# Performance work log

Hardware: AMD Instinct MI355X
Metric: run time of the kernel (lower is better)

## Reference

```python
import jax, jax.numpy as jnp
import numpy as np

SHAPES = ((64, 64), (32, 32), (16, 16), (8, 8))
LEVEL_STARTS = np.concatenate([[0], np.cumsum([h * w for h, w in SHAPES])]).tolist()
N_LEVELS = 4; N_HEADS = 8; N_POINTS = 4; D_MODEL = 256; HEAD_DIM = 32; D_FFN = 1024; NUM_LAYERS = 2
LEN_IN = sum(h * w for h, w in SHAPES)
BATCH = 2


def setup_inputs():
    key = jax.random.key(0)
    ks = iter(jax.random.split(key, 40))
    r = lambda shape, s=1.0: jax.random.normal(next(ks), shape, dtype=jnp.float32) * s
    L = NUM_LAYERS
    return {
        "src": r((BATCH, LEN_IN, D_MODEL)),
        "pos": r((BATCH, LEN_IN, D_MODEL), 0.5),
        "valid_ratios": jnp.ones((BATCH, N_LEVELS, 2), jnp.float32),
        "Wv": r((L, D_MODEL, D_MODEL), 0.05), "bv": jnp.zeros((L, D_MODEL), jnp.float32),
        "Woff": r((L, D_MODEL, N_HEADS * N_LEVELS * N_POINTS * 2), 0.002),
        "boff": r((L, N_HEADS * N_LEVELS * N_POINTS * 2), 0.5),
        "Wa": r((L, D_MODEL, N_HEADS * N_LEVELS * N_POINTS), 0.05),
        "ba": jnp.zeros((L, N_HEADS * N_LEVELS * N_POINTS), jnp.float32),
        "Wo": r((L, D_MODEL, D_MODEL), 0.05), "bo": jnp.zeros((L, D_MODEL), jnp.float32),
        "g1": jnp.ones((L, D_MODEL), jnp.float32), "be1": jnp.zeros((L, D_MODEL), jnp.float32),
        "Wl1": r((L, D_MODEL, D_FFN), 0.05), "bl1": jnp.zeros((L, D_FFN), jnp.float32),
        "Wl2": r((L, D_FFN, D_MODEL), 0.05), "bl2": jnp.zeros((L, D_MODEL), jnp.float32),
        "g2": jnp.ones((L, D_MODEL), jnp.float32), "be2": jnp.zeros((L, D_MODEL), jnp.float32),
    }


def layer_norm(x, g, b, eps=1e-5):
    m = jnp.mean(x, -1, keepdims=True)
    v = jnp.mean(jnp.square(x - m), -1, keepdims=True)
    return (x - m) * jax.lax.rsqrt(v + eps) * g + b


def make_reference_points(valid_ratios):
    # DeformableTransformerEncoder.get_reference_points, vectorized per level
    refs = []
    for lvl, (H, W) in enumerate(SHAPES):
        gy, gx = jnp.meshgrid(jnp.arange(H, dtype=jnp.float32) + 0.5,
                              jnp.arange(W, dtype=jnp.float32) + 0.5, indexing="ij")
        ry = gy.reshape(-1)[None] / (valid_ratios[:, lvl, 1][:, None] * H)
        rx = gx.reshape(-1)[None] / (valid_ratios[:, lvl, 0][:, None] * W)
        refs.append(jnp.stack([rx, ry], -1))  # [N, H*W, 2]
    ref = jnp.concatenate(refs, 1)  # [N, Len, 2]
    return ref[:, :, None, :] * valid_ratios[:, None]  # [N, Len, n_levels, 2]


def ms_deform_attn(query, input_flatten, reference_points, Wv, bv, Woff, boff, Wa, ba, Wo, bo):
    N, Lq, _ = query.shape
    value = (input_flatten @ Wv + bv).reshape(N, -1, N_HEADS, HEAD_DIM)
    off = (query @ Woff + boff).reshape(N, Lq, N_HEADS, N_LEVELS, N_POINTS, 2)
    aw = (query @ Wa + ba).reshape(N, Lq, N_HEADS, N_LEVELS * N_POINTS)
    aw = jax.nn.softmax(aw, -1).reshape(N, Lq, N_HEADS, N_LEVELS, N_POINTS)
    # normalizer is (W, H) per level, as in MSDeformAttn
    normalizer = jnp.array([[w, h] for h, w in SHAPES], jnp.float32)
    loc = reference_points[:, :, None, :, None, :] + off / normalizer[None, None, None, :, None, :]
    acc = jnp.zeros((N, N_HEADS, Lq, HEAD_DIM), query.dtype)
    for lvl, (H, W) in enumerate(SHAPES):
        s = LEVEL_STARTS[lvl]
        val = value[:, s:s + H * W].transpose(0, 2, 1, 3)  # [N, heads, H*W, hd]
        # grid_sample bilinear, align_corners=False, zero padding
        x = loc[:, :, :, lvl, :, 0] * W - 0.5  # [N, Lq, heads, P]
        y = loc[:, :, :, lvl, :, 1] * H - 0.5
        x0 = jnp.floor(x); y0 = jnp.floor(y)
        wx1 = x - x0; wy1 = y - y0
        ix0 = x0.astype(jnp.int32); iy0 = y0.astype(jnp.int32)

        def corner(ix, iy, w):
            valid = (ix >= 0) & (ix < W) & (iy >= 0) & (iy < H)
            idx = jnp.clip(iy, 0, H - 1) * W + jnp.clip(ix, 0, W - 1)
            idx = idx.transpose(0, 2, 1, 3).reshape(N, N_HEADS, Lq * N_POINTS)
            g = jnp.take_along_axis(val, idx[..., None], axis=2).reshape(N, N_HEADS, Lq, N_POINTS, HEAD_DIM)
            w = jnp.where(valid, w, 0.0).transpose(0, 2, 1, 3)  # [N, heads, Lq, P]
            return g * w[..., None]

        sampled = (corner(ix0, iy0, (1 - wx1) * (1 - wy1))
                   + corner(ix0 + 1, iy0, wx1 * (1 - wy1))
                   + corner(ix0, iy0 + 1, (1 - wx1) * wy1)
                   + corner(ix0 + 1, iy0 + 1, wx1 * wy1))
        acc = acc + (sampled * aw[:, :, :, lvl].transpose(0, 2, 1, 3)[..., None]).sum(3)
    out = acc.transpose(0, 2, 1, 3).reshape(N, Lq, D_MODEL)
    return out @ Wo + bo


def reference(src, pos, valid_ratios, Wv, bv, Woff, boff, Wa, ba, Wo, bo,
              g1, be1, Wl1, bl1, Wl2, bl2, g2, be2):
    ref_pts = make_reference_points(valid_ratios)
    out = src
    for l in range(NUM_LAYERS):
        q = out + pos  # with_pos_embed
        attn = ms_deform_attn(q, out, ref_pts, Wv[l], bv[l], Woff[l], boff[l],
                              Wa[l], ba[l], Wo[l], bo[l])
        out = layer_norm(out + attn, g1[l], be1[l])
        ffn = jax.nn.relu(out @ Wl1[l] + bl1[l]) @ Wl2[l] + bl2[l]
        out = layer_norm(out + ffn, g2[l], be2[l])
    return out
```

## Files before the change

kernel.cpp:

```cpp
#include <hip/hip_runtime.h>
#include <math.h>

#define LEN   5440
#define NB    2
#define MROWS (NB * LEN)
#define DM    256
#define NH    8
#define HD    32
#define NLV   4
#define NPT   4
#define DFFN  1024

typedef __attribute__((ext_vector_type(8))) short bf16x8;
typedef __attribute__((ext_vector_type(4))) short bf16x4;
typedef __attribute__((ext_vector_type(4))) float f32x4;

#define MFMA16 __builtin_amdgcn_mfma_f32_16x16x32_bf16

__device__ __forceinline__ short f2bf(float f) {
    union { float f; unsigned u; } cv; cv.f = f;
    unsigned r = cv.u + 0x7fffu + ((cv.u >> 16) & 1u);
    return (short)(r >> 16);
}
__device__ __forceinline__ float bf2f(short s) {
    union { unsigned u; float f; } cv;
    cv.u = ((unsigned)(unsigned short)s) << 16;
    return cv.f;
}

__device__ __forceinline__ void gload16(const short* g, short* l) {
    __builtin_amdgcn_global_load_lds(
        (__attribute__((address_space(1))) void*)g,
        (__attribute__((address_space(3))) void*)l, 16, 0, 0);
}

template <int N> __device__ __forceinline__ void vmwait();
template <> __device__ __forceinline__ void vmwait<0>() { asm volatile("s_waitcnt vmcnt(0)" ::: "memory"); }
template <> __device__ __forceinline__ void vmwait<4>() { asm volatile("s_waitcnt vmcnt(4)" ::: "memory"); }
template <> __device__ __forceinline__ void vmwait<5>() { asm volatile("s_waitcnt vmcnt(5)" ::: "memory"); }

__device__ __forceinline__ int swz(int row) { return (row >> 1) & 3; }

__global__ __launch_bounds__(256) void transpose_convert_all(
    const float* __restrict__ Wv,  const float* __restrict__ Woff,
    const float* __restrict__ Wa,  const float* __restrict__ Wo,
    const float* __restrict__ Wl1, const float* __restrict__ Wl2,
    short* __restrict__ out)
{
    int bx = blockIdx.x;
    int l  = bx / 736;
    int t  = bx % 736;
    const float* src; int K, N; long doff;
    if      (t < 64)  { src = Wv;   K = 256;  N = 256;  doff = 0;      }
    else if (t < 128) { src = Woff; K = 256;  N = 256;  doff = 65536;  t -= 64;  }
    else if (t < 160) { src = Wa;   K = 256;  N = 128;  doff = 131072; t -= 128; }
    else if (t < 224) { src = Wo;   K = 256;  N = 256;  doff = 163840; t -= 160; }
    else if (t < 480) { src = Wl1;  K = 256;  N = 1024; doff = 229376; t -= 224; }
    else              { src = Wl2;  K = 1024; N = 256;  doff = 491520; t -= 480; }
    src += (long)l * K * N;
    short* dst = out + (long)l * 753664 + doff;

    const int ntx = N / 32;
    const int n0 = (t % ntx) * 32, k0 = (t / ntx) * 32;

    __shared__ short T[32][33];
    const int tid = threadIdx.x;
    {
        const int n = tid & 31, kq = tid >> 5;
        #pragma unroll
        for (int i = 0; i < 4; ++i) {
            int k = kq * 4 + i;
            T[n][k] = f2bf(src[(long)(k0 + k) * N + n0 + n]);
        }
    }
    __syncthreads();
    {
        const int k = tid & 31, nq = tid >> 5;
        #pragma unroll
        for (int i = 0; i < 4; ++i) {
            int n = nq * 4 + i;
            dst[(long)(n0 + n) * K + k0 + k] = T[n][k];
        }
    }
}

__global__ __launch_bounds__(256) void convert_src(
    const float4* __restrict__ s4, const float4* __restrict__ p4,
    bf16x4* __restrict__ curb, bf16x4* __restrict__ qb)
{
    const int i = blockIdx.x * 256 + threadIdx.x;
    float4 s = s4[i], p = p4[i];
    bf16x4 c, q;
    c[0] = f2bf(s.x); c[1] = f2bf(s.y); c[2] = f2bf(s.z); c[3] = f2bf(s.w);
    q[0] = f2bf(s.x + p.x); q[1] = f2bf(s.y + p.y);
    q[2] = f2bf(s.z + p.z); q[3] = f2bf(s.w + p.w);
    curb[i] = c; qb[i] = q;
}

template <int RELU, int OMODE, int K>
__device__ __forceinline__ void gemm_core128_v2(
    short* As, short* Bs,
    const short* __restrict__ A, const short* __restrict__ Wt,
    const float* __restrict__ bias, float* __restrict__ Cf,
    short* __restrict__ Cb, int ldc, int m0, int wrow0, int ccol0)
{
    constexpr int NT = K / 32;
    static_assert(NT >= 4 && (NT & 1) == 0, "NT even >= 4");
    const int t    = threadIdx.x;
    const int wave = t >> 6, lane = t & 63;
    const int wm   = (wave & 1) * 64;
    const int wn   = (wave >> 1) * 64;
    const int lm   = lane & 15;
    const int chkg = lane >> 4;

    const short* aS[2]; const short* bS[2];
    short *aD[2], *bD[2];
    #pragma unroll
    for (int i = 0; i < 2; ++i) {
        const int c   = wave * 2 + i;
        const int row = c * 16 + (lane >> 2);
        const int xc  = (lane & 3) ^ swz(row);
        aS[i] = A  + (long)(m0 + row) * K + xc * 8;
        bS[i] = Wt + (long)(wrow0 + row) * K + xc * 8;
        aD[i] = As + c * 512;
        bD[i] = Bs + c * 512;
    }

    int offA[4], offB[4];
    #pragma unroll
    for (int s = 0; s < 4; ++s) {
        const int r = wm + s * 16 + lm;
        offA[s] = r * 32 + (chkg ^ swz(r)) * 8;
    }
    #pragma unroll
    for (int u = 0; u < 4; ++u) {
        const int r = wn + u * 16 + lm;
        offB[u] = r * 32 + (chkg ^ swz(r)) * 8;
    }

    f32x4 acc[4][4] = {};

#define STG128(BUF, KT) do {                                          \
        const int _ko = (KT) * 32;                                    \
        gload16(aS[0] + _ko, aD[0] + (BUF) * 4096);                   \
        gload16(bS[0] + _ko, bD[0] + (BUF) * 4096);                   \
        gload16(aS[1] + _ko, aD[1] + (BUF) * 4096);                   \
        gload16(bS[1] + _ko, bD[1] + (BUF) * 4096);                   \
    } while (0)

#define GB128(T, BUF, WN, DOSTAGE) do {                               \
        vmwait<WN>();                     \
        __builtin_amdgcn_s_barrier();     \
        bf16x8 af[4], bv[4];                                          \
        _Pragma("unroll")                                             \
        for (int s = 0; s < 4; ++s)                                   \
            af[s] = *(const bf16x8*)(As + (BUF) * 4096 + offA[s]);    \
        _Pragma("unroll")                                             \
        for (int u = 0; u < 4; ++u)                                   \
            bv[u] = *(const bf16x8*)(Bs + (BUF) * 4096 + offB[u]);    \
        asm volatile("s_waitcnt lgkmcnt(0)" ::: "memory");            \
        __builtin_amdgcn_s_barrier();     \
        __builtin_amdgcn_sched_barrier(0);                            \
        if (DOSTAGE) STG128(BUF, (T) + 2);                            \
        _Pragma("unroll")                                             \
        for (int s = 0; s < 4; ++s)                                   \
            _Pragma("unroll")                                         \
            for (int u = 0; u < 4; ++u)                               \
                acc[s][u] = MFMA16(af[s], bv[u], acc[s][u], 0, 0, 0); \
    } while (0)

    STG128(0, 0);
    STG128(1, 1);
    for (int tt = 0; tt < NT - 2; tt += 2) {
        GB128(tt,     0, 4, true);
        GB128(tt + 1, 1, 4, true);
    }
    GB128(NT - 2, 0, 4, false);
    GB128(NT - 1, 1, 0, false);
#undef GB128
#undef STG128

    const int col = lane & 15;
    const int rq  = (lane >> 4) * 4;
    #pragma unroll
    for (int s = 0; s < 4; ++s) {
        #pragma unroll
        for (int u = 0; u < 4; ++u) {
            const int gn = ccol0 + wn + u * 16 + col;
            const float bb = bias[gn];
            #pragma unroll
            for (int r = 0; r < 4; ++r) {
                const int gm = m0 + wm + s * 16 + rq + r;
                float v = acc[s][u][r] + bb;
                if (RELU) v = fmaxf(v, 0.f);
                if (OMODE == 0) {
                    Cf[(long)gm * ldc + gn] = v;
                } else if (OMODE == 1) {
                    Cb[(long)gm * ldc + gn] = f2bf(v);
                } else {
                    const int n   = gm / LEN;
                    const int pix = gm - n * LEN;
                    const int h   = gn >> 5, d = gn & 31;
                    Cb[((long)(n * NH + h) * LEN + pix) * 32 + d] = f2bf(v);
                }
            }
        }
    }
}

template <int RELU, int OMODE, int K>
__global__ __launch_bounds__(256) void gemm128v2(
    const short* __restrict__ A, const short* __restrict__ Wt,
    const float* __restrict__ bias, float* Cf, short* Cb, int ldc)
{
    __shared__ __align__(16) short As[2 * 128 * 32];
    __shared__ __align__(16) short Bs[2 * 128 * 32];
    gemm_core128_v2<RELU, OMODE, K>(As, Bs, A, Wt, bias, Cf, Cb, ldc,
                                    blockIdx.y * 128, blockIdx.x * 128,
                                    blockIdx.x * 128);
}

__global__ __launch_bounds__(256) void gemm_qkv128(
    const short* __restrict__ curb, const short* __restrict__ qb,
    const short* __restrict__ Wt, const float* __restrict__ bv,
    const float* __restrict__ boff, const float* __restrict__ ba,
    short* __restrict__ Vb, float* __restrict__ OFF, float* __restrict__ AW)
{
    __shared__ __align__(16) short As[2 * 128 * 32];
    __shared__ __align__(16) short Bs[2 * 128 * 32];
    const int n0 = blockIdx.x * 128;
    if (n0 < 256) {
        gemm_core128_v2<0, 2, 256>(As, Bs, curb, Wt, bv, (float*)nullptr, Vb,
                                   256, blockIdx.y * 128, n0, n0);
    } else if (n0 < 512) {
        gemm_core128_v2<0, 0, 256>(As, Bs, qb, Wt, boff, OFF, (short*)nullptr,
                                   256, blockIdx.y * 128, n0, n0 - 256);
    } else {
        gemm_core128_v2<0, 0, 256>(As, Bs, qb, Wt, ba, AW, (short*)nullptr,
                                   128, blockIdx.y * 128, n0, n0 - 512);
    }
}

template <int K>
__global__ __launch_bounds__(256) void gemm_ln(
    const short* __restrict__ A, const short* __restrict__ Wt,
    const float* __restrict__ bias, const short* __restrict__ residb,
    const float* __restrict__ g, const float* __restrict__ be,
    short* __restrict__ outb, short* __restrict__ outq,
    float* __restrict__ outf, const float* __restrict__ pos)
{
    constexpr int NT = K / 32;
    __shared__ __align__(16) short As[2 * 32 * 32];
    __shared__ __align__(16) short Bs[2 * 256 * 32];
    __shared__ float red[2][32][2];

    const int t    = threadIdx.x;
    const int wave = t >> 6, lane = t & 63;
    const int wm   = (wave & 1) * 16;
    const int wn   = (wave >> 1) * 128;
    const int lm   = lane & 15;
    const int chkg = lane >> 4;
    const int rq   = chkg * 4;
    const int m0   = blockIdx.x * 32;
    const bool hasA = (wave & 1) == 0;

    short rr[8][4];
    #pragma unroll
    for (int u = 0; u < 8; ++u)
        #pragma unroll
        for (int r = 0; r < 4; ++r)
            rr[u][r] = residb[(long)(m0 + wm + rq + r) * DM + wn + u * 16 + lm];
    asm volatile("" ::: "memory");

    const short* bSp[4]; short* bDp[4];
    #pragma unroll
    for (int i = 0; i < 4; ++i) {
        const int c   = wave * 4 + i;
        const int row = c * 16 + (lane >> 2);
        const int xc  = (lane & 3) ^ swz(row);
        bSp[i] = Wt + (long)row * K + xc * 8;
        bDp[i] = Bs + c * 512;
    }
    const short* aSp = nullptr; short* aDp = nullptr;
    if (hasA) {
        const int c   = wave >> 1;
        const int row = c * 16 + (lane >> 2);
        const int xc  = (lane & 3) ^ swz(row);
        aSp = A + (long)(m0 + row) * K + xc * 8;
        aDp = As + c * 512;
    }

    const int offA = (wm + lm) * 32 + (chkg ^ swz(wm + lm)) * 8;
    int offB[8];
    #pragma unroll
    for (int u = 0; u < 8; ++u) {
        const int r = wn + u * 16 + lm;
        offB[u] = r * 32 + (chkg ^ swz(r)) * 8;
    }

    f32x4 acc[8] = {};

#define STGLN(BUF, KT) do {                                           \
        const int _ko = (KT) * 32;                                    \
        if (hasA) gload16(aSp + _ko, aDp + (BUF) * 1024);             \
        gload16(bSp[0] + _ko, bDp[0] + (BUF) * 8192);                 \
        gload16(bSp[1] + _ko, bDp[1] + (BUF) * 8192);                 \
        gload16(bSp[2] + _ko, bDp[2] + (BUF) * 8192);                 \
        gload16(bSp[3] + _ko, bDp[3] + (BUF) * 8192);                 \
    } while (0)

#define GBLN(T, BUF, WA, WB, DOSTAGE) do {                            \
        if (hasA) vmwait<WA>(); else vmwait<WB>();                    \
        __builtin_amdgcn_s_barrier();                                 \
        bf16x8 af = *(const bf16x8*)(As + (BUF) * 1024 + offA);       \
        bf16x8 bv[8];                                                 \
        _Pragma("unroll")                                             \
        for (int u = 0; u < 8; ++u)                                   \
            bv[u] = *(const bf16x8*)(Bs + (BUF) * 8192 + offB[u]);    \
        asm volatile("s_waitcnt lgkmcnt(0)" ::: "memory");            \
        __builtin_amdgcn_s_barrier();                                 \
        __builtin_amdgcn_sched_barrier(0);                            \
        if (DOSTAGE) STGLN(BUF, (T) + 2);                             \
        _Pragma("unroll")                                             \
        for (int u = 0; u < 8; ++u)                                   \
            acc[u] = MFMA16(af, bv[u], acc[u], 0, 0, 0);              \
    } while (0)

    STGLN(0, 0);
    STGLN(1, 1);
    for (int tt = 0; tt < NT - 2; tt += 2) {
        GBLN(tt,     0, 5, 4, true);
        GBLN(tt + 1, 1, 5, 4, true);
    }
    GBLN(NT - 2, 0, 5, 4, false);
    GBLN(NT - 1, 1, 0, 0, false);
#undef GBLN
#undef STGLN

    #pragma unroll
    for (int u = 0; u < 8; ++u) {
        const int gn = wn + u * 16 + lm;
        const float bb = bias[gn];
        #pragma unroll
        for (int r = 0; r < 4; ++r)
            acc[u][r] += bb + bf2f(rr[u][r]);
    }

    float rs[4], r2[4];
    #pragma unroll
    for (int r = 0; r < 4; ++r) {
        float s = 0.f, s2 = 0.f;
        #pragma unroll
        for (int u = 0; u < 8; ++u) { const float v = acc[u][r]; s += v; s2 += v * v; }
        rs[r] = s; r2[r] = s2;
    }
    #pragma unroll
    for (int o = 1; o < 16; o <<= 1)
        #pragma unroll
        for (int r = 0; r < 4; ++r) {
            rs[r] += __shfl_xor(rs[r], o, 64);
            r2[r] += __shfl_xor(r2[r], o, 64);
        }
    if (lm == 0) {
        #pragma unroll
        for (int r = 0; r < 4; ++r) {
            red[wave >> 1][wm + rq + r][0] = rs[r];
            red[wave >> 1][wm + rq + r][1] = r2[r];
        }
    }
    __syncthreads();
    #pragma unroll
    for (int r = 0; r < 4; ++r) {
        const int row = wm + rq + r;
        const float ts = red[0][row][0] + red[1][row][0];
        const float t2 = red[0][row][1] + red[1][row][1];
        const float mean = ts * (1.f / DM);
        const float var  = t2 * (1.f / DM) - mean * mean;
        rs[r] = mean;
        r2[r] = rsqrtf(var + 1e-5f);
    }
    #pragma unroll
    for (int u = 0; u < 8; ++u) {
        const int gn = wn + u * 16 + lm;
        const float gg = g[gn], bbe = be[gn];
        #pragma unroll
        for (int r = 0; r < 4; ++r) {
            const long gm = m0 + wm + rq + r;
            const float o = (acc[u][r] - rs[r]) * r2[r] * gg + bbe;
            if (outb) outb[gm * DM + gn] = f2bf(o);
            if (outq) outq[gm * DM + gn] = f2bf(o + pos[gm * DM + gn]);
            if (outf) outf[gm * DM + gn] = o;
        }
    }
}

__global__ __launch_bounds__(256) void deform_attn_v3(
    const short* __restrict__ Vb,
    const float* __restrict__ OFF,
    const float* __restrict__ AW,
    const float* __restrict__ vr,
    bf16x4* __restrict__ ATTb)
{
    const int starts[5] = {0, 4096, 5120, 5376, 5440};
    const int dims[4]   = {64, 32, 16, 8};

    const int wave = threadIdx.x >> 6;
    const int lane = threadIdx.x & 63;
    const int h    = lane >> 3;
    const int d4   = lane & 7;

    const int gq = blockIdx.x * 4 + wave;
    const int n  = gq / LEN;
    const int q  = gq % LEN;

    int lq = 3;
    if (q < 4096) lq = 0; else if (q < 5120) lq = 1; else if (q < 5376) lq = 2;
    const int r  = q - starts[lq];
    const int Wq = dims[lq];
    const int gy = r / Wq, gx = r % Wq;
    const float vrxq = vr[(n * NLV + lq) * 2 + 0];
    const float vryq = vr[(n * NLV + lq) * 2 + 1];
    const float rx = (gx + 0.5f) / (vrxq * Wq);
    const float ry = (gy + 0.5f) / (vryq * Wq);

    const long row = (long)n * LEN + q;

    const float* awp = AW + row * 128 + h * 16;
    float a[16];
    float mx = -1e30f;
    #pragma unroll
    for (int i = 0; i < 16; ++i) { a[i] = awp[i]; mx = fmaxf(mx, a[i]); }
    float s = 0.f;
    #pragma unroll
    for (int i = 0; i < 16; ++i) { a[i] = __expf(a[i] - mx); s += a[i]; }
    const float inv = 1.f / s;

    const float* offp = OFF + row * 256 + h * 32;

    float4 acc = {0.f, 0.f, 0.f, 0.f};
    #pragma unroll
    for (int lvl = 0; lvl < NLV; ++lvl) {
        const int Hl = dims[lvl];
        const int Wl = Hl;
        const float fW = (float)Wl;
        const int sb = starts[lvl];
        const float lx = rx * vr[(n * NLV + lvl) * 2 + 0];
        const float ly = ry * vr[(n * NLV + lvl) * 2 + 1];
        const short* vb = Vb + ((long)(n * NH + h) * LEN + sb) * 32 + d4 * 4;
        #pragma unroll
        for (int p = 0; p < NPT; ++p) {
            const float ox = offp[lvl * 8 + p * 2 + 0];
            const float oy = offp[lvl * 8 + p * 2 + 1];
            const float x = fmaf(lx, fW, ox) - 0.5f;
            const float y = fmaf(ly, fW, oy) - 0.5f;
            const float x0f = floorf(x), y0f = floorf(y);
            const int ix0 = (int)x0f, iy0 = (int)y0f;
            const float wx1 = x - x0f, wy1 = y - y0f;
            const float wx0 = 1.f - wx1, wy0 = 1.f - wy1;

            const bool vx0 = (ix0 >= 0)     && (ix0 < Wl);
            const bool vx1 = (ix0 + 1 >= 0) && (ix0 + 1 < Wl);
            const bool vy0 = (iy0 >= 0)     && (iy0 < Hl);
            const bool vy1 = (iy0 + 1 >= 0) && (iy0 + 1 < Hl);
            const int cx0 = min(max(ix0, 0), Wl - 1);
            const int cx1 = min(max(ix0 + 1, 0), Wl - 1);
            const int cy0 = min(max(iy0, 0), Hl - 1);
            const int cy1 = min(max(iy0 + 1, 0), Hl - 1);

            const float w00 = (vx0 && vy0) ? wx0 * wy0 : 0.f;
            const float w10 = (vx1 && vy0) ? wx1 * wy0 : 0.f;
            const float w01 = (vx0 && vy1) ? wx0 * wy1 : 0.f;
            const float w11 = (vx1 && vy1) ? wx1 * wy1 : 0.f;

            const bf16x4 g00 = *(const bf16x4*)(vb + (long)(cy0 * Wl + cx0) * 32);
            const bf16x4 g10 = *(const bf16x4*)(vb + (long)(cy0 * Wl + cx1) * 32);
            const bf16x4 g01 = *(const bf16x4*)(vb + (long)(cy1 * Wl + cx0) * 32);
            const bf16x4 g11 = *(const bf16x4*)(vb + (long)(cy1 * Wl + cx1) * 32);

            const float awv = a[lvl * 4 + p] * inv;
            #pragma unroll
            for (int e = 0; e < 4; ++e) {
                float sv = w00 * bf2f(g00[e]) + w10 * bf2f(g10[e])
                         + w01 * bf2f(g01[e]) + w11 * bf2f(g11[e]);
                (&acc.x)[e] += awv * sv;
            }
        }
    }
    bf16x4 ob;
    ob[0] = f2bf(acc.x); ob[1] = f2bf(acc.y);
    ob[2] = f2bf(acc.z); ob[3] = f2bf(acc.w);
    ATTb[row * 64 + h * 8 + d4] = ob;
}

extern "C" void kernel_launch(void* const* d_in, const int* in_sizes, int n_in,
                              void* d_out, int out_size, void* d_ws, size_t ws_size,
                              hipStream_t stream)
{
    const float* src = (const float*)d_in[0];
    const float* pos = (const float*)d_in[1];
    const float* vr  = (const float*)d_in[2];
    const float* Wv_   = (const float*)d_in[3];
    const float* bv_   = (const float*)d_in[4];
    const float* Woff_ = (const float*)d_in[5];
    const float* boff_ = (const float*)d_in[6];
    const float* Wa_   = (const float*)d_in[7];
    const float* ba_   = (const float*)d_in[8];
    const float* Wo_   = (const float*)d_in[9];
    const float* bo_   = (const float*)d_in[10];
    const float* g1_   = (const float*)d_in[11];
    const float* be1_  = (const float*)d_in[12];
    const float* Wl1_  = (const float*)d_in[13];
    const float* bl1_  = (const float*)d_in[14];
    const float* Wl2_  = (const float*)d_in[15];
    const float* bl2_  = (const float*)d_in[16];
    const float* g2_   = (const float*)d_in[17];
    const float* be2_  = (const float*)d_in[18];

    const long SZ = (long)MROWS * DM;
    float* ws = (float*)d_ws;
    float* OFF  = ws;
    float* AW   = OFF + SZ;
    short* Vb   = (short*)(AW + (long)MROWS * 128);
    short* curb = Vb   + SZ;
    short* qb   = curb + SZ;
    short* ATTb = qb   + SZ;
    short* XAb  = ATTb + SZ;
    short* FFNb = XAb  + SZ;
    short* Wt   = FFNb + (long)MROWS * DFFN;

    const dim3 blk(256);
    const int GYM = MROWS / 128;
    const int GLN = MROWS / 32;

    hipLaunchKernelGGL(transpose_convert_all, dim3(1472), blk, 0, stream,
                       Wv_, Woff_, Wa_, Wo_, Wl1_, Wl2_, Wt);
    hipLaunchKernelGGL(convert_src, dim3(SZ / 4 / 256), blk, 0, stream,
                       (const float4*)src, (const float4*)pos,
                       (bf16x4*)curb, (bf16x4*)qb);

    for (int l = 0; l < 2; ++l) {
        const short* Wbase = Wt + (long)l * 753664;
        const float* bv   = bv_   + (long)l * DM;
        const float* boff = boff_ + (long)l * 256;
        const float* ba   = ba_   + (long)l * 128;
        const float* bo   = bo_   + (long)l * DM;
        const float* g1   = g1_   + (long)l * DM;
        const float* be1  = be1_  + (long)l * DM;
        const float* bl1  = bl1_  + (long)l * DFFN;
        const float* bl2  = bl2_  + (long)l * DM;
        const float* g2   = g2_   + (long)l * DM;
        const float* be2  = be2_  + (long)l * DM;

        hipLaunchKernelGGL(gemm_qkv128, dim3(5, GYM), blk, 0, stream,
                           curb, qb, Wbase, bv, boff, ba, Vb, OFF, AW);
        hipLaunchKernelGGL(deform_attn_v3, dim3(MROWS / 4), blk, 0, stream,
                           Vb, OFF, AW, vr, (bf16x4*)ATTb);
        hipLaunchKernelGGL((gemm_ln<256>), dim3(GLN), blk, 0, stream,
                           ATTb, Wbase + 163840, bo, curb, g1, be1,
                           XAb, (short*)nullptr, (float*)nullptr,
                           (const float*)nullptr);
        hipLaunchKernelGGL((gemm128v2<1, 1, 256>), dim3(8, GYM), blk, 0, stream,
                           XAb, Wbase + 229376, bl1, (float*)nullptr, FFNb, 1024);
        if (l == 0) {
            hipLaunchKernelGGL((gemm_ln<1024>), dim3(GLN), blk, 0, stream,
                               FFNb, Wbase + 491520, bl2, XAb, g2, be2,
                               curb, qb, (float*)nullptr, pos);
        } else {
            hipLaunchKernelGGL((gemm_ln<1024>), dim3(GLN), blk, 0, stream,
                               FFNb, Wbase + 491520, bl2, XAb, g2, be2,
                               (short*)nullptr, (short*)nullptr,
                               (float*)d_out, (const float*)nullptr);
        }
    }
}
```

Before: 291.9 us.

## Use 4-slot LDS ring with register double-buffering in GEMM main loops; merge prep kernels

```diff
diff --git a/kernel.cpp b/kernel.cpp
--- a/kernel.cpp
+++ b/kernel.cpp
@@ -39,14 +39,32 @@
 template <> __device__ __forceinline__ void vmwait<4>() { asm volatile("s_waitcnt vmcnt(4)" ::: "memory"); }
 template <> __device__ __forceinline__ void vmwait<5>() { asm volatile("s_waitcnt vmcnt(5)" ::: "memory"); }
 
+template <int N> __device__ __forceinline__ void lgkwait();
+template <> __device__ __forceinline__ void lgkwait<0>() { asm volatile("s_waitcnt lgkmcnt(0)" ::: "memory"); }
+template <> __device__ __forceinline__ void lgkwait<8>() { asm volatile("s_waitcnt lgkmcnt(8)" ::: "memory"); }
+template <> __device__ __forceinline__ void lgkwait<9>() { asm volatile("s_waitcnt lgkmcnt(9)" ::: "memory"); }
+
 __device__ __forceinline__ int swz(int row) { return (row >> 1) & 3; }
 
-__global__ __launch_bounds__(256) void transpose_convert_all(
+__global__ __launch_bounds__(256) void prep_all(
     const float* __restrict__ Wv,  const float* __restrict__ Woff,
     const float* __restrict__ Wa,  const float* __restrict__ Wo,
     const float* __restrict__ Wl1, const float* __restrict__ Wl2,
-    short* __restrict__ out)
+    short* __restrict__ out,
+    const float4* __restrict__ s4, const float4* __restrict__ p4,
+    bf16x4* __restrict__ curb, bf16x4* __restrict__ qb)
 {
+    __shared__ short T[32][33];
+    if (blockIdx.x >= 1472) {
+        const int i = (blockIdx.x - 1472) * 256 + threadIdx.x;
+        float4 s = s4[i], p = p4[i];
+        bf16x4 c, q;
+        c[0] = f2bf(s.x); c[1] = f2bf(s.y); c[2] = f2bf(s.z); c[3] = f2bf(s.w);
+        q[0] = f2bf(s.x + p.x); q[1] = f2bf(s.y + p.y);
+        q[2] = f2bf(s.z + p.z); q[3] = f2bf(s.w + p.w);
+        curb[i] = c; qb[i] = q;
+        return;
+    }
     int bx = blockIdx.x;
     int l  = bx / 736;
     int t  = bx % 736;
@@ -63,7 +81,6 @@
     const int ntx = N / 32;
     const int n0 = (t % ntx) * 32, k0 = (t / ntx) * 32;
 
-    __shared__ short T[32][33];
     const int tid = threadIdx.x;
     {
         const int n = tid & 31, kq = tid >> 5;
@@ -84,28 +101,15 @@
     }
 }
 
-__global__ __launch_bounds__(256) void convert_src(
-    const float4* __restrict__ s4, const float4* __restrict__ p4,
-    bf16x4* __restrict__ curb, bf16x4* __restrict__ qb)
-{
-    const int i = blockIdx.x * 256 + threadIdx.x;
-    float4 s = s4[i], p = p4[i];
-    bf16x4 c, q;
-    c[0] = f2bf(s.x); c[1] = f2bf(s.y); c[2] = f2bf(s.z); c[3] = f2bf(s.w);
-    q[0] = f2bf(s.x + p.x); q[1] = f2bf(s.y + p.y);
-    q[2] = f2bf(s.z + p.z); q[3] = f2bf(s.w + p.w);
-    curb[i] = c; qb[i] = q;
-}
-
 template <int RELU, int OMODE, int K>
-__device__ __forceinline__ void gemm_core128_v2(
+__device__ __forceinline__ void gemm_core128_v3(
     short* As, short* Bs,
     const short* __restrict__ A, const short* __restrict__ Wt,
     const float* __restrict__ bias, float* __restrict__ Cf,
     short* __restrict__ Cb, int ldc, int m0, int wrow0, int ccol0)
 {
     constexpr int NT = K / 32;
-    static_assert(NT >= 4 && (NT & 1) == 0, "NT even >= 4");
+    static_assert(NT >= 4, "NT >= 4");
     const int t    = threadIdx.x;
     const int wave = t >> 6, lane = t & 63;
     const int wm   = (wave & 1) * 64;
@@ -139,46 +143,56 @@
     }
 
     f32x4 acc[4][4] = {};
-
-#define STG128(BUF, KT) do {                                          \
+    bf16x8 afr[2][4], bfr[2][4];
+
+#define STG3(KT) do {                                                 \
+        const int _b  = ((KT) & 3) * 4096;                            \
         const int _ko = (KT) * 32;                                    \
-        gload16(aS[0] + _ko, aD[0] + (BUF) * 4096);                   \
-        gload16(bS[0] + _ko, bD[0] + (BUF) * 4096);                   \
-        gload16(aS[1] + _ko, aD[1] + (BUF) * 4096);                   \
-        gload16(bS[1] + _ko, bD[1] + (BUF) * 4096);                   \
+        gload16(aS[0] + _ko, aD[0] + _b);                             \
+        gload16(bS[0] + _ko, bD[0] + _b);                             \
+        gload16(aS[1] + _ko, aD[1] + _b);                             \
+        gload16(bS[1] + _ko, bD[1] + _b);                             \
     } while (0)
 
-#define GB128(T, BUF, WN, DOSTAGE) do {                               \
-        vmwait<WN>();                     \
-        __builtin_amdgcn_s_barrier();     \
-        bf16x8 af[4], bv[4];                                          \
+#define RD3(SET, KT) do {                                             \
+        const int _b = ((KT) & 3) * 4096;                             \
         _Pragma("unroll")                                             \
         for (int s = 0; s < 4; ++s)                                   \
-            af[s] = *(const bf16x8*)(As + (BUF) * 4096 + offA[s]);    \
+            afr[SET][s] = *(const bf16x8*)(As + _b + offA[s]);        \
         _Pragma("unroll")                                             \
         for (int u = 0; u < 4; ++u)                                   \
-            bv[u] = *(const bf16x8*)(Bs + (BUF) * 4096 + offB[u]);    \
-        asm volatile("s_waitcnt lgkmcnt(0)" ::: "memory");            \
-        __builtin_amdgcn_s_barrier();     \
-        __builtin_amdgcn_sched_barrier(0);                            \
-        if (DOSTAGE) STG128(BUF, (T) + 2);                            \
-        _Pragma("unroll")                                             \
-        for (int s = 0; s < 4; ++s)                                   \
-            _Pragma("unroll")                                         \
-            for (int u = 0; u < 4; ++u)                               \
-                acc[s][u] = MFMA16(af[s], bv[u], acc[s][u], 0, 0, 0); \
+            bfr[SET][u] = *(const bf16x8*)(Bs + _b + offB[u]);        \
     } while (0)
 
-    STG128(0, 0);
-    STG128(1, 1);
-    for (int tt = 0; tt < NT - 2; tt += 2) {
-        GB128(tt,     0, 4, true);
-        GB128(tt + 1, 1, 4, true);
-    }
-    GB128(NT - 2, 0, 4, false);
-    GB128(NT - 1, 1, 0, false);
-#undef GB128
-#undef STG128
+    STG3(0);
+    STG3(1);
+    vmwait<4>();
+    __builtin_amdgcn_s_barrier();
+    RD3(0, 0);
+
+    #pragma unroll
+    for (int kt = 0; kt < NT; ++kt) {
+        if (kt + 2 < NT) STG3(kt + 2);
+        if (kt + 1 < NT) {
+            if (kt + 2 < NT) vmwait<4>(); else vmwait<0>();
+            __builtin_amdgcn_s_barrier();
+            RD3((kt + 1) & 1, kt + 1);
+            lgkwait<8>();
+        } else {
+            lgkwait<0>();
+        }
+        __builtin_amdgcn_sched_barrier(0);
+        __builtin_amdgcn_s_setprio(1);
+        const int cs = kt & 1;
+        #pragma unroll
+        for (int s = 0; s < 4; ++s)
+            #pragma unroll
+            for (int u = 0; u < 4; ++u)
+                acc[s][u] = MFMA16(afr[cs][s], bfr[cs][u], acc[s][u], 0, 0, 0);
+        __builtin_amdgcn_s_setprio(0);
+    }
+#undef RD3
+#undef STG3
 
     const int col = lane & 15;
     const int rq  = (lane >> 4) * 4;
@@ -209,13 +223,13 @@
 }
 
 template <int RELU, int OMODE, int K>
-__global__ __launch_bounds__(256) void gemm128v2(
+__global__ __launch_bounds__(256) void gemm128v3(
     const short* __restrict__ A, const short* __restrict__ Wt,
     const float* __restrict__ bias, float* Cf, short* Cb, int ldc)
 {
-    __shared__ __align__(16) short As[2 * 128 * 32];
-    __shared__ __align__(16) short Bs[2 * 128 * 32];
-    gemm_core128_v2<RELU, OMODE, K>(As, Bs, A, Wt, bias, Cf, Cb, ldc,
+    __shared__ __align__(16) short As[4 * 128 * 32];
+    __shared__ __align__(16) short Bs[4 * 128 * 32];
+    gemm_core128_v3<RELU, OMODE, K>(As, Bs, A, Wt, bias, Cf, Cb, ldc,
                                     blockIdx.y * 128, blockIdx.x * 128,
                                     blockIdx.x * 128);
 }
@@ -226,17 +240,17 @@
     const float* __restrict__ boff, const float* __restrict__ ba,
     short* __restrict__ Vb, float* __restrict__ OFF, float* __restrict__ AW)
 {
-    __shared__ __align__(16) short As[2 * 128 * 32];
-    __shared__ __align__(16) short Bs[2 * 128 * 32];
+    __shared__ __align__(16) short As[4 * 128 * 32];
+    __shared__ __align__(16) short Bs[4 * 128 * 32];
     const int n0 = blockIdx.x * 128;
     if (n0 < 256) {
-        gemm_core128_v2<0, 2, 256>(As, Bs, curb, Wt, bv, (float*)nullptr, Vb,
+        gemm_core128_v3<0, 2, 256>(As, Bs, curb, Wt, bv, (float*)nullptr, Vb,
                                    256, blockIdx.y * 128, n0, n0);
     } else if (n0 < 512) {
-        gemm_core128_v2<0, 0, 256>(As, Bs, qb, Wt, boff, OFF, (short*)nullptr,
+        gemm_core128_v3<0, 0, 256>(As, Bs, qb, Wt, boff, OFF, (short*)nullptr,
                                    256, blockIdx.y * 128, n0, n0 - 256);
     } else {
-        gemm_core128_v2<0, 0, 256>(As, Bs, qb, Wt, ba, AW, (short*)nullptr,
+        gemm_core128_v3<0, 0, 256>(As, Bs, qb, Wt, ba, AW, (short*)nullptr,
                                    128, blockIdx.y * 128, n0, n0 - 512);
     }
 }
@@ -250,8 +264,8 @@
     float* __restrict__ outf, const float* __restrict__ pos)
 {
     constexpr int NT = K / 32;
-    __shared__ __align__(16) short As[2 * 32 * 32];
-    __shared__ __align__(16) short Bs[2 * 256 * 32];
+    __shared__ __align__(16) short As[4 * 32 * 32];
+    __shared__ __align__(16) short Bs[4 * 256 * 32];
     __shared__ float red[2][32][2];
 
     const int t    = threadIdx.x;
@@ -299,43 +313,56 @@
     }
 
     f32x4 acc[8] = {};
-
-#define STGLN(BUF, KT) do {                                           \
+    bf16x8 afr[2], bfr[2][8];
+
+#define STGL(KT) do {                                                 \
+        const int _ba = ((KT) & 3) * 1024;                            \
+        const int _bb = ((KT) & 3) * 8192;                            \
         const int _ko = (KT) * 32;                                    \
-        if (hasA) gload16(aSp + _ko, aDp + (BUF) * 1024);             \
-        gload16(bSp[0] + _ko, bDp[0] + (BUF) * 8192);                 \
-        gload16(bSp[1] + _ko, bDp[1] + (BUF) * 8192);                 \
-        gload16(bSp[2] + _ko, bDp[2] + (BUF) * 8192);                 \
-        gload16(bSp[3] + _ko, bDp[3] + (BUF) * 8192);                 \
+        if (hasA) gload16(aSp + _ko, aDp + _ba);                      \
+        gload16(bSp[0] + _ko, bDp[0] + _bb);                          \
+        gload16(bSp[1] + _ko, bDp[1] + _bb);                          \
+        gload16(bSp[2] + _ko, bDp[2] + _bb);                          \
+        gload16(bSp[3] + _ko, bDp[3] + _bb);                          \
     } while (0)
 
-#define GBLN(T, BUF, WA, WB, DOSTAGE) do {                            \
-        if (hasA) vmwait<WA>(); else vmwait<WB>();                    \
-        __builtin_amdgcn_s_barrier();                                 \
-        bf16x8 af = *(const bf16x8*)(As + (BUF) * 1024 + offA);       \
-        bf16x8 bv[8];                                                 \
+#define RDL(SET, KT) do {                                             \
+        const int _ba = ((KT) & 3) * 1024;                            \
+        const int _bb = ((KT) & 3) * 8192;                            \
+        afr[SET] = *(const bf16x8*)(As + _ba + offA);                 \
         _Pragma("unroll")                                             \
         for (int u = 0; u < 8; ++u)                                   \
-            bv[u] = *(const bf16x8*)(Bs + (BUF) * 8192 + offB[u]);    \
-        asm volatile("s_waitcnt lgkmcnt(0)" ::: "memory");            \
-        __builtin_amdgcn_s_barrier();                                 \
-        __builtin_amdgcn_sched_barrier(0);                            \
-        if (DOSTAGE) STGLN(BUF, (T) + 2);                             \
-        _Pragma("unroll")                                             \
-        for (int u = 0; u < 8; ++u)                                   \
-            acc[u] = MFMA16(af, bv[u], acc[u], 0, 0, 0);              \
+            bfr[SET][u] = *(const bf16x8*)(Bs + _bb + offB[u]);       \
     } while (0)
 
-    STGLN(0, 0);
-    STGLN(1, 1);
-    for (int tt = 0; tt < NT - 2; tt += 2) {
-        GBLN(tt,     0, 5, 4, true);
-        GBLN(tt + 1, 1, 5, 4, true);
-    }
-    GBLN(NT - 2, 0, 5, 4, false);
-    GBLN(NT - 1, 1, 0, 0, false);
-#undef GBLN
-#undef STGLN
+    STGL(0);
+    STGL(1);
+    if (hasA) vmwait<5>(); else vmwait<4>();
+    __builtin_amdgcn_s_barrier();
+    RDL(0, 0);
+
+    #pragma unroll
+    for (int kt = 0; kt < NT; ++kt) {
+        if (kt + 2 < NT) STGL(kt + 2);
+        if (kt + 1 < NT) {
+            if (kt + 2 < NT) { if (hasA) vmwait<5>(); else vmwait<4>(); }
+            else             vmwait<0>();
+            __builtin_amdgcn_s_barrier();
+            RDL((kt + 1) & 1, kt + 1);
+            lgkwait<9>();
+        } else {
+            lgkwait<0>();
+        }
+        __builtin_amdgcn_sched_barrier(0);
+        __builtin_amdgcn_s_setprio(1);
+        const int cs = kt & 1;
+        #pragma unroll
+        for (int u = 0; u < 8; ++u)
+            acc[u] = MFMA16(afr[cs], bfr[cs][u], acc[u], 0, 0, 0);
+        __builtin_amdgcn_s_setprio(0);
+    }
+#undef RDL
+#undef STGL
 
     #pragma unroll
     for (int u = 0; u < 8; ++u) {
@@ -532,9 +559,8 @@
     const int GYM = MROWS / 128;
     const int GLN = MROWS / 32;
 
-    hipLaunchKernelGGL(transpose_convert_all, dim3(1472), blk, 0, stream,
-                       Wv_, Woff_, Wa_, Wo_, Wl1_, Wl2_, Wt);
-    hipLaunchKernelGGL(convert_src, dim3(SZ / 4 / 256), blk, 0, stream,
+    hipLaunchKernelGGL(prep_all, dim3(1472 + SZ / 4 / 256), blk, 0, stream,
+                       Wv_, Woff_, Wa_, Wo_, Wl1_, Wl2_, Wt,
                        (const float4*)src, (const float4*)pos,
                        (bf16x4*)curb, (bf16x4*)qb);
 
@@ -559,7 +585,7 @@
                            ATTb, Wbase + 163840, bo, curb, g1, be1,
                            XAb, (short*)nullptr, (float*)nullptr,
                            (const float*)nullptr);
-        hipLaunchKernelGGL((gemm128v2<1, 1, 256>), dim3(8, GYM), blk, 0, stream,
+        hipLaunchKernelGGL((gemm128v3<1, 1, 256>), dim3(8, GYM), blk, 0, stream,
                            XAb, Wbase + 229376, bl1, (float*)nullptr, FFNb, 1024);
         if (l == 0) {
             hipLaunchKernelGGL((gemm_ln<1024>), dim3(GLN), blk, 0, stream,
```

Measured after the change: 297.4 us. Within noise of the previous version (+1.9%).

## Split-K the FFN second GEMM with separate LayerNorm finalize; merge prep kernels

Applied to the files above, without the earlier changes.

```diff
diff --git a/kernel.cpp b/kernel.cpp
--- a/kernel.cpp
+++ b/kernel.cpp
@@ -41,12 +41,25 @@
 
 __device__ __forceinline__ int swz(int row) { return (row >> 1) & 3; }
 
-__global__ __launch_bounds__(256) void transpose_convert_all(
+__global__ __launch_bounds__(256) void prep_all(
     const float* __restrict__ Wv,  const float* __restrict__ Woff,
     const float* __restrict__ Wa,  const float* __restrict__ Wo,
     const float* __restrict__ Wl1, const float* __restrict__ Wl2,
-    short* __restrict__ out)
-{
+    short* __restrict__ out,
+    const float4* __restrict__ s4, const float4* __restrict__ p4,
+    bf16x4* __restrict__ curb, bf16x4* __restrict__ qb)
+{
+    __shared__ short T[32][33];
+    if (blockIdx.x >= 1472) {
+        const int i = (blockIdx.x - 1472) * 256 + threadIdx.x;
+        float4 s = s4[i], p = p4[i];
+        bf16x4 c, q;
+        c[0] = f2bf(s.x); c[1] = f2bf(s.y); c[2] = f2bf(s.z); c[3] = f2bf(s.w);
+        q[0] = f2bf(s.x + p.x); q[1] = f2bf(s.y + p.y);
+        q[2] = f2bf(s.z + p.z); q[3] = f2bf(s.w + p.w);
+        curb[i] = c; qb[i] = q;
+        return;
+    }
     int bx = blockIdx.x;
     int l  = bx / 736;
     int t  = bx % 736;
@@ -63,7 +76,6 @@
     const int ntx = N / 32;
     const int n0 = (t % ntx) * 32, k0 = (t / ntx) * 32;
 
-    __shared__ short T[32][33];
     const int tid = threadIdx.x;
     {
         const int n = tid & 31, kq = tid >> 5;
@@ -82,19 +94,6 @@
             dst[(long)(n0 + n) * K + k0 + k] = T[n][k];
         }
     }
-}
-
-__global__ __launch_bounds__(256) void convert_src(
-    const float4* __restrict__ s4, const float4* __restrict__ p4,
-    bf16x4* __restrict__ curb, bf16x4* __restrict__ qb)
-{
-    const int i = blockIdx.x * 256 + threadIdx.x;
-    float4 s = s4[i], p = p4[i];
-    bf16x4 c, q;
-    c[0] = f2bf(s.x); c[1] = f2bf(s.y); c[2] = f2bf(s.z); c[3] = f2bf(s.w);
-    q[0] = f2bf(s.x + p.x); q[1] = f2bf(s.y + p.y);
-    q[2] = f2bf(s.z + p.z); q[3] = f2bf(s.w + p.w);
-    curb[i] = c; qb[i] = q;
 }
 
 template <int RELU, int OMODE, int K>
@@ -149,8 +148,8 @@
     } while (0)
 
 #define GB128(T, BUF, WN, DOSTAGE) do {                               \
-        vmwait<WN>();                     \
-        __builtin_amdgcn_s_barrier();     \
+        vmwait<WN>();                                                 \
+        __builtin_amdgcn_s_barrier();                                 \
         bf16x8 af[4], bv[4];                                          \
         _Pragma("unroll")                                             \
         for (int s = 0; s < 4; ++s)                                   \
@@ -159,7 +158,7 @@
         for (int u = 0; u < 4; ++u)                                   \
             bv[u] = *(const bf16x8*)(Bs + (BUF) * 4096 + offB[u]);    \
         asm volatile("s_waitcnt lgkmcnt(0)" ::: "memory");            \
-        __builtin_amdgcn_s_barrier();     \
+        __builtin_amdgcn_s_barrier();                                 \
         __builtin_amdgcn_sched_barrier(0);                            \
         if (DOSTAGE) STG128(BUF, (T) + 2);                            \
         _Pragma("unroll")                                             \
@@ -300,7 +299,7 @@
 
     f32x4 acc[8] = {};
 
-#define STGLN(BUF, KT) do {                                           \
+#define STGL(BUF, KT) do {                                            \
         const int _ko = (KT) * 32;                                    \
         if (hasA) gload16(aSp + _ko, aDp + (BUF) * 1024);             \
         gload16(bSp[0] + _ko, bDp[0] + (BUF) * 8192);                 \
@@ -320,14 +319,14 @@
         asm volatile("s_waitcnt lgkmcnt(0)" ::: "memory");            \
         __builtin_amdgcn_s_barrier();                                 \
         __builtin_amdgcn_sched_barrier(0);                            \
-        if (DOSTAGE) STGLN(BUF, (T) + 2);                             \
+        if (DOSTAGE) STGL(BUF, (T) + 2);                              \
         _Pragma("unroll")                                             \
         for (int u = 0; u < 8; ++u)                                   \
             acc[u] = MFMA16(af, bv[u], acc[u], 0, 0, 0);              \
     } while (0)
 
-    STGLN(0, 0);
-    STGLN(1, 1);
+    STGL(0, 0);
+    STGL(1, 1);
     for (int tt = 0; tt < NT - 2; tt += 2) {
         GBLN(tt,     0, 5, 4, true);
         GBLN(tt + 1, 1, 5, 4, true);
@@ -335,7 +334,7 @@
     GBLN(NT - 2, 0, 5, 4, false);
     GBLN(NT - 1, 1, 0, 0, false);
 #undef GBLN
-#undef STGLN
+#undef STGL
 
     #pragma unroll
     for (int u = 0; u < 8; ++u) {
@@ -390,6 +389,163 @@
             if (outb) outb[gm * DM + gn] = f2bf(o);
             if (outq) outq[gm * DM + gn] = f2bf(o + pos[gm * DM + gn]);
             if (outf) outf[gm * DM + gn] = o;
+        }
+    }
+}
+
+template <int KLEN, int KSTR>
+__global__ __launch_bounds__(256) void ln2_part_k(
+    const short* __restrict__ A0, const short* __restrict__ Wt0,
+    float* __restrict__ PART)
+{
+    constexpr int NT = KLEN / 32;
+    static_assert(NT >= 4 && (NT & 1) == 0, "NT even >= 4");
+    __shared__ __align__(16) short As[2 * 32 * 32];
+    __shared__ __align__(16) short Bs[2 * 256 * 32];
+
+    const int kk = blockIdx.x;
+    const int m0 = blockIdx.y * 32;
+    const short* A  = A0  + kk * KLEN;
+    const short* Wt = Wt0 + kk * KLEN;
+    float* Pout = PART + (long)kk * MROWS * DM;
+
+    const int t    = threadIdx.x;
+    const int wave = t >> 6, lane = t & 63;
+    const int wm   = (wave & 1) * 16;
+    const int wn   = (wave >> 1) * 128;
+    const int lm   = lane & 15;
+    const int chkg = lane >> 4;
+    const int rq   = chkg * 4;
+    const bool hasA = (wave & 1) == 0;
+
+    const short* bSp[4]; short* bDp[4];
+    #pragma unroll
+    for (int i = 0; i < 4; ++i) {
+        const int c   = wave * 4 + i;
+        const int row = c * 16 + (lane >> 2);
+        const int xc  = (lane & 3) ^ swz(row);
+        bSp[i] = Wt + (long)row * KSTR + xc * 8;
+        bDp[i] = Bs + c * 512;
+    }
+    const short* aSp = nullptr; short* aDp = nullptr;
+    if (hasA) {
+        const int c   = wave >> 1;
+        const int row = c * 16 + (lane >> 2);
+        const int xc  = (lane & 3) ^ swz(row);
+        aSp = A + (long)(m0 + row) * KSTR + xc * 8;
+        aDp = As + c * 512;
+    }
+
+    const int offA = (wm + lm) * 32 + (chkg ^ swz(wm + lm)) * 8;
+    int offB[8];
+    #pragma unroll
+    for (int u = 0; u < 8; ++u) {
+        const int r = wn + u * 16 + lm;
+        offB[u] = r * 32 + (chkg ^ swz(r)) * 8;
+    }
+
+    f32x4 acc[8] = {};
+
+#define STGP(BUF, KT) do {                                            \
+        const int _ko = (KT) * 32;                                    \
+        if (hasA) gload16(aSp + _ko, aDp + (BUF) * 1024);             \
+        gload16(bSp[0] + _ko, bDp[0] + (BUF) * 8192);                 \
+        gload16(bSp[1] + _ko, bDp[1] + (BUF) * 8192);                 \
+        gload16(bSp[2] + _ko, bDp[2] + (BUF) * 8192);                 \
+        gload16(bSp[3] + _ko, bDp[3] + (BUF) * 8192);                 \
+    } while (0)
+
+#define GBP(T, BUF, WA, WB, DOSTAGE) do {                             \
+        if (hasA) vmwait<WA>(); else vmwait<WB>();                    \
+        __builtin_amdgcn_s_barrier();                                 \
+        bf16x8 af = *(const bf16x8*)(As + (BUF) * 1024 + offA);       \
+        bf16x8 bv[8];                                                 \
+        _Pragma("unroll")                                             \
+        for (int u = 0; u < 8; ++u)                                   \
+            bv[u] = *(const bf16x8*)(Bs + (BUF) * 8192 + offB[u]);    \
+        asm volatile("s_waitcnt lgkmcnt(0)" ::: "memory");            \
+        __builtin_amdgcn_s_barrier();                                 \
+        __builtin_amdgcn_sched_barrier(0);                            \
+        if (DOSTAGE) STGP(BUF, (T) + 2);                              \
+        _Pragma("unroll")                                             \
+        for (int u = 0; u < 8; ++u)                                   \
+            acc[u] = MFMA16(af, bv[u], acc[u], 0, 0, 0);              \
+    } while (0)
+
+    STGP(0, 0);
+    STGP(1, 1);
+    for (int tt = 0; tt < NT - 2; tt += 2) {
+        GBP(tt,     0, 5, 4, true);
+        GBP(tt + 1, 1, 5, 4, true);
+    }
+    GBP(NT - 2, 0, 5, 4, false);
+    GBP(NT - 1, 1, 0, 0, false);
+#undef GBP
+#undef STGP
+
+    #pragma unroll
+    for (int u = 0; u < 8; ++u) {
+        const int gn = wn + u * 16 + lm;
+        #pragma unroll
+        for (int r = 0; r < 4; ++r)
+            Pout[(long)(m0 + wm + rq + r) * DM + gn] = acc[u][r];
+    }
+}
+
+__global__ __launch_bounds__(256) void ln2_fin_k(
+    const float* __restrict__ PART, const short* __restrict__ residb,
+    const float* __restrict__ bl2, const float* __restrict__ g,
+    const float* __restrict__ be, short* __restrict__ outb,
+    short* __restrict__ outq, float* __restrict__ outf,
+    const float* __restrict__ pos)
+{
+    const int wave = threadIdx.x >> 6, lane = threadIdx.x & 63;
+    const int c0 = lane * 4;
+    const f32x4 bb = *(const f32x4*)(bl2 + c0);
+    const f32x4 gg = *(const f32x4*)(g + c0);
+    const f32x4 ee = *(const f32x4*)(be + c0);
+    #pragma unroll 1
+    for (int r = 0; r < 8; ++r) {
+        const long row = (long)blockIdx.x * 32 + wave * 8 + r;
+        const f32x4 p0 = *(const f32x4*)(PART + row * DM + c0);
+        const f32x4 p1 = *(const f32x4*)(PART + (long)MROWS * DM + row * DM + c0);
+        const bf16x4 rr = *(const bf16x4*)(residb + row * DM + c0);
+        float v[4]; float s = 0.f, s2 = 0.f;
+        #pragma unroll
+        for (int j = 0; j < 4; ++j) {
+            v[j] = p0[j] + p1[j] + bb[j] + bf2f(rr[j]);
+            s += v[j]; s2 += v[j] * v[j];
+        }
+        #pragma unroll
+        for (int o = 1; o < 64; o <<= 1) {
+            s  += __shfl_xor(s,  o, 64);
+            s2 += __shfl_xor(s2, o, 64);
+        }
+        const float mean = s * (1.f / DM);
+        const float var  = s2 * (1.f / DM) - mean * mean;
+        const float rstd = rsqrtf(var + 1e-5f);
+        float o4[4];
+        #pragma unroll
+        for (int j = 0; j < 4; ++j)
+            o4[j] = (v[j] - mean) * rstd * gg[j] + ee[j];
+        if (outb) {
+            bf16x4 ob;
+            #pragma unroll
+            for (int j = 0; j < 4; ++j) ob[j] = f2bf(o4[j]);
+            *(bf16x4*)(outb + row * DM + c0) = ob;
+        }
+        if (outq) {
+            const f32x4 pp = *(const f32x4*)(pos + row * DM + c0);
+            bf16x4 oq;
+            #pragma unroll
+            for (int j = 0; j < 4; ++j) oq[j] = f2bf(o4[j] + pp[j]);
+            *(bf16x4*)(outq + row * DM + c0) = oq;
+        }
+        if (outf) {
+            f32x4 of;
+            #pragma unroll
+            for (int j = 0; j < 4; ++j) of[j] = o4[j];
+            *(f32x4*)(outf + row * DM + c0) = of;
         }
     }
 }
@@ -527,14 +683,14 @@
     short* XAb  = ATTb + SZ;
     short* FFNb = XAb  + SZ;
     short* Wt   = FFNb + (long)MROWS * DFFN;
+    float* PART = (float*)(Wt + 2L * 753664);
 
     const dim3 blk(256);
     const int GYM = MROWS / 128;
     const int GLN = MROWS / 32;
 
-    hipLaunchKernelGGL(transpose_convert_all, dim3(1472), blk, 0, stream,
-                       Wv_, Woff_, Wa_, Wo_, Wl1_, Wl2_, Wt);
-    hipLaunchKernelGGL(convert_src, dim3(SZ / 4 / 256), blk, 0, stream,
+    hipLaunchKernelGGL(prep_all, dim3(1472 + SZ / 4 / 256), blk, 0, stream,
+                       Wv_, Woff_, Wa_, Wo_, Wl1_, Wl2_, Wt,
                        (const float4*)src, (const float4*)pos,
                        (bf16x4*)curb, (bf16x4*)qb);
 
@@ -561,13 +717,15 @@
                            (const float*)nullptr);
         hipLaunchKernelGGL((gemm128v2<1, 1, 256>), dim3(8, GYM), blk, 0, stream,
                            XAb, Wbase + 229376, bl1, (float*)nullptr, FFNb, 1024);
+        hipLaunchKernelGGL((ln2_part_k<512, 1024>), dim3(2, GLN), blk, 0, stream,
+                           FFNb, Wbase + 491520, PART);
         if (l == 0) {
-            hipLaunchKernelGGL((gemm_ln<1024>), dim3(GLN), blk, 0, stream,
-                               FFNb, Wbase + 491520, bl2, XAb, g2, be2,
+            hipLaunchKernelGGL(ln2_fin_k, dim3(GLN), blk, 0, stream,
+                               PART, XAb, bl2, g2, be2,
                                curb, qb, (float*)nullptr, pos);
         } else {
-            hipLaunchKernelGGL((gemm_ln<1024>), dim3(GLN), blk, 0, stream,
-                               FFNb, Wbase + 491520, bl2, XAb, g2, be2,
+            hipLaunchKernelGGL(ln2_fin_k, dim3(GLN), blk, 0, stream,
+                               PART, XAb, bl2, g2, be2,
                                (short*)nullptr, (short*)nullptr,
                                (float*)d_out, (const float*)nullptr);
         }
```

Result: no change. 293.8 us (+0.6%).
